# Optimization experiments

Hardware: AMD Instinct MI355X
Metric: run time of the kernel (lower is better)

Reference implementation:

```python
import jax, jax.numpy as jnp
import numpy as np

B = 2
L = 1024
D_MODEL = 1024
D_INNER = 2048   # expand * d_model
D_STATE = 16
DT_RANK = 64     # ceil(d_model / 16)
D_CONV = 4


def setup_inputs() -> dict:
    key = jax.random.key(0)
    ks = jax.random.split(key, 8)
    def nrm(k, shape, scale):
        return jax.random.normal(k, shape, dtype=jnp.float32) * scale
    A_log = jnp.log(jnp.tile(jnp.arange(1, D_STATE + 1, dtype=jnp.float32)[None, :], (D_INNER, 1)))
    return dict(
        hidden_states=jax.random.normal(ks[0], (B, L, D_MODEL), dtype=jnp.float32),
        Win=nrm(ks[1], (D_MODEL, 2 * D_INNER), D_MODEL ** -0.5),
        Wx=nrm(ks[2], (D_INNER, DT_RANK + 2 * D_STATE), D_INNER ** -0.5),
        Wdt=nrm(ks[3], (DT_RANK, D_INNER), DT_RANK ** -0.5),
        dt_bias=nrm(ks[4], (D_INNER,), 1.0),
        Wout=nrm(ks[5], (D_INNER, D_MODEL), D_INNER ** -0.5),
        dw_kernel=nrm(ks[6], (D_CONV, D_INNER), 0.2),
        dw_bias=jnp.zeros((D_INNER,), dtype=jnp.float32),
        A_log=A_log,
        Dskip=jnp.ones((D_INNER,), dtype=jnp.float32),
    )


def _causal_depthwise_conv(x, kernel, bias):
    # x: (B, L, D_INNER), kernel: (k, D_INNER); dilation 1, causal left pad
    k = kernel.shape[0]
    Lq = x.shape[1]
    xpad = jnp.pad(x, ((0, 0), (k - 1, 0), (0, 0)))
    y = sum(xpad[:, i:i + Lq, :] * kernel[i] for i in range(k)) + bias
    return jax.nn.silu(y)


def _selective_scan(u, delta, A, Bm, Cm, Dskip, z):
    # u, delta, z: (B, L, D); A: (D, N); Bm, Cm: (B, L, N)
    deltaA = jnp.exp(jnp.einsum('bld,dn->bldn', delta, A))      # (B,L,D,N)
    deltaBu = jnp.einsum('bld,bln,bld->bldn', delta, Bm, u)     # (B,L,D,N)

    def step(x_prev, elems):
        dA, dBu, c = elems                                      # (B,D,N),(B,D,N),(B,N)
        x_new = dA * x_prev + dBu
        y = jnp.einsum('bdn,bn->bd', x_new, c)
        return x_new, y

    x0 = jnp.zeros((u.shape[0], u.shape[2], A.shape[1]), dtype=jnp.float32)
    _, ys = jax.lax.scan(
        step, x0,
        (deltaA.transpose(1, 0, 2, 3), deltaBu.transpose(1, 0, 2, 3), Cm.transpose(1, 0, 2)))
    y = ys.transpose(1, 0, 2) + u * Dskip                        # skip connection
    return y * jax.nn.silu(z)


def reference(hidden_states, Win, Wx, Wdt, dt_bias, Wout, dw_kernel, dw_bias, A_log, Dskip):
    xz = hidden_states @ Win                                     # (B,L,2*D_INNER)
    x, z = jnp.split(xz, 2, axis=-1)
    A = -jnp.exp(A_log)                                          # (D_INNER, D_STATE)
    x = _causal_depthwise_conv(x, dw_kernel, dw_bias)
    x_dbl = x @ Wx                                               # (B,L,DT_RANK+2*N)
    dt, Bm, Cm = jnp.split(x_dbl, [DT_RANK, DT_RANK + D_STATE], axis=-1)
    delta = jax.nn.softplus(dt @ Wdt + dt_bias)                  # delta_bias + softplus
    y = _selective_scan(x, delta, A, Bm, Cm, Dskip, z)
    return y @ Wout
```

## Files before the change

### kernel.cpp

```cpp
#include <hip/hip_runtime.h>
#include <hip/hip_bf16.h>
#include <math.h>

#define B_SZ 2
#define L_SZ 1024
#define DM 1024
#define DI 2048
#define NS 16
#define DTR 64
#define NCHUNK 16
#define CLEN 64
#define XDLD 128
#define KSPLIT 16

typedef unsigned short ushortT;
typedef __attribute__((ext_vector_type(8))) short short8;
typedef __attribute__((ext_vector_type(4))) float floatx4;

__device__ __forceinline__ ushortT f2bf(float f) {
  unsigned u = __float_as_uint(f);
  unsigned r = (u + 0x7fff + ((u >> 16) & 1)) >> 16;
  return (ushortT)r;
}

__device__ __forceinline__ float bf2f(ushortT v) {
  return __uint_as_float((unsigned)v << 16);
}

__device__ __forceinline__ void gl2lds16(const void* g, void* l) {
  __builtin_amdgcn_global_load_lds(
      (const __attribute__((address_space(1))) unsigned int*)g,
      (__attribute__((address_space(3))) unsigned int*)l, 16, 0, 0);
}

__device__ __forceinline__ unsigned stash_addr(unsigned i) {
  return (i >> 10) * 4096 + 1024 + (i & 1023);
}

__global__ __launch_bounds__(256) void cvt_bf16(const float* __restrict__ src,
                                                ushortT* __restrict__ dst) {
  const int i = blockIdx.x * 256 + threadIdx.x;
  float4 v = ((const float4*)src)[i];
  unsigned lo = (unsigned)f2bf(v.x) | ((unsigned)f2bf(v.y) << 16);
  unsigned hi = (unsigned)f2bf(v.z) | ((unsigned)f2bf(v.w) << 16);
  ((uint2*)dst)[i] = make_uint2(lo, hi);
}

__global__ __launch_bounds__(256) void transpose_bf16(
    const float* __restrict__ src, ushortT* __restrict__ dst, int R, int C) {
  __shared__ float t[32][33];
  const int bx = blockIdx.x * 32;
  const int by = blockIdx.y * 32;
  const int tx = threadIdx.x, ty = threadIdx.y;
#pragma unroll
  for (int j = 0; j < 4; ++j)
    t[ty + j * 8][tx] = src[(size_t)(by + ty + j * 8) * C + bx + tx];
  __syncthreads();
#pragma unroll
  for (int j = 0; j < 4; ++j)
    dst[(size_t)(bx + ty + j * 8) * R + by + tx] = f2bf(t[tx][ty + j * 8]);
}

__global__ __launch_bounds__(256) void wx_pad_t(const float* __restrict__ Wx,
                                                ushortT* __restrict__ WxT) {
  const int k = blockIdx.x * 256 + threadIdx.x;
  const int n = blockIdx.y;
  WxT[(size_t)n * DI + k] = (n < 96) ? f2bf(Wx[(size_t)k * 96 + n]) : (ushortT)0;
}

__global__ __launch_bounds__(512) void gemm1_big(
    const ushortT* __restrict__ A, int lda,
    const ushortT* __restrict__ BT, int ldb,
    float* __restrict__ C, int ldc, int K) {
  __shared__ __align__(16) char smem[128 * 128 + 128 * 128];
  char* As = smem;
  char* Bs = smem + 128 * 128;
  const int tid = threadIdx.x;
  const int lane = tid & 63;
  const int quad = lane >> 4;
  const int l16 = lane & 15;
  const int wid = tid >> 6;
  const int wm = wid & 1;
  const int wn = wid >> 1;
  const int m0 = blockIdx.y * 128;
  const int n0 = blockIdx.x * 128;

  floatx4 acc[4][2] = {};

  for (int k0 = 0; k0 < K; k0 += 64) {
    for (int i = tid; i < 128 * 8; i += 512) {
      const int r = i >> 3, c = i & 7;
      const int cg = c ^ (r & 7);
      gl2lds16(A + (size_t)(m0 + r) * lda + k0 + cg * 8, As + (i - lane) * 16);
    }
    for (int i = tid; i < 128 * 8; i += 512) {
      const int r = i >> 3, c = i & 7;
      const int cg = c ^ (r & 7);
      gl2lds16(BT + (size_t)(n0 + r) * ldb + k0 + cg * 8, Bs + (i - lane) * 16);
    }
    __syncthreads();

    short8 afr[4][2], bfr[2][2];
#pragma unroll
    for (int i = 0; i < 4; ++i) {
      const int r = wm * 64 + i * 16 + l16;
#pragma unroll
      for (int s = 0; s < 2; ++s)
        afr[i][s] = *(const short8*)(As + r * 128 + (((s * 4 + quad) ^ (r & 7)) * 16));
    }
#pragma unroll
    for (int j = 0; j < 2; ++j) {
      const int r = wn * 32 + j * 16 + l16;
#pragma unroll
      for (int s = 0; s < 2; ++s)
        bfr[j][s] = *(const short8*)(Bs + r * 128 + (((s * 4 + quad) ^ (r & 7)) * 16));
    }
#pragma unroll
    for (int s = 0; s < 2; ++s)
#pragma unroll
      for (int i = 0; i < 4; ++i)
#pragma unroll
        for (int j = 0; j < 2; ++j)
          acc[i][j] = __builtin_amdgcn_mfma_f32_16x16x32_bf16(afr[i][s], bfr[j][s],
                                                              acc[i][j], 0, 0, 0);
    __syncthreads();
  }
#pragma unroll
  for (int i = 0; i < 4; ++i)
#pragma unroll
    for (int j = 0; j < 2; ++j)
#pragma unroll
      for (int r = 0; r < 4; ++r) {
        const int m = m0 + wm * 64 + i * 16 + quad * 4 + r;
        const int n = n0 + wn * 32 + j * 16 + l16;
        C[(size_t)m * ldc + n] = acc[i][j][r];
      }
}

__global__ __launch_bounds__(256) void gemm_out_split(
    const ushortT* __restrict__ A, int lda,
    const ushortT* __restrict__ BT, int ldb,
    float* __restrict__ part) {
  __shared__ __align__(16) char smem[64 * 128 + 64 * 128];
  char* As = smem;
  char* Bs = smem + 64 * 128;
  const int tid = threadIdx.x;
  const int lane = tid & 63;
  const int quad = lane >> 4;
  const int l16 = lane & 15;
  const int wid = tid >> 6;
  const int wm = wid & 1;
  const int wn = wid >> 1;
  const int m0 = blockIdx.y * 64;
  const int n0 = blockIdx.x * 64;
  const int kb = blockIdx.z * (DI / 2);

  floatx4 acc[2][2] = {};

  for (int k0 = kb; k0 < kb + DI / 2; k0 += 64) {
    for (int i = tid; i < 64 * 8; i += 256) {
      const int r = i >> 3, c = i & 7;
      const int cg = c ^ (r & 7);
      gl2lds16(A + (size_t)(m0 + r) * lda + k0 + cg * 8, As + (i - lane) * 16);
    }
    for (int i = tid; i < 64 * 8; i += 256) {
      const int r = i >> 3, c = i & 7;
      const int cg = c ^ (r & 7);
      gl2lds16(BT + (size_t)(n0 + r) * ldb + k0 + cg * 8, Bs + (i - lane) * 16);
    }
    __syncthreads();

    short8 afr[2][2], bfr[2][2];
#pragma unroll
    for (int i = 0; i < 2; ++i) {
      const int m = wm * 32 + i * 16 + l16;
#pragma unroll
      for (int s = 0; s < 2; ++s)
        afr[i][s] = *(const short8*)(As + m * 128 + (((s * 4 + quad) ^ (m & 7)) * 16));
    }
#pragma unroll
    for (int j = 0; j < 2; ++j) {
      const int n = wn * 32 + j * 16 + l16;
#pragma unroll
      for (int s = 0; s < 2; ++s)
        bfr[j][s] = *(const short8*)(Bs + n * 128 + (((s * 4 + quad) ^ (n & 7)) * 16));
    }
#pragma unroll
    for (int s = 0; s < 2; ++s)
#pragma unroll
      for (int i = 0; i < 2; ++i)
#pragma unroll
        for (int j = 0; j < 2; ++j)
          acc[i][j] = __builtin_amdgcn_mfma_f32_16x16x32_bf16(afr[i][s], bfr[j][s],
                                                              acc[i][j], 0, 0, 0);
    __syncthreads();
  }
  float* out = part + (size_t)blockIdx.z * (B_SZ * L_SZ * DM);
#pragma unroll
  for (int i = 0; i < 2; ++i)
#pragma unroll
    for (int j = 0; j < 2; ++j)
#pragma unroll
      for (int r = 0; r < 4; ++r) {
        const int m = m0 + wm * 32 + i * 16 + quad * 4 + r;
        const int n = n0 + wn * 32 + j * 16 + l16;
        out[(size_t)m * DM + n] = acc[i][j][r];
      }
}

__global__ __launch_bounds__(256) void reduce_out(const float* __restrict__ part,
                                                  float* __restrict__ out) {
  const int i = blockIdx.x * 256 + threadIdx.x;
  const float4 a = ((const float4*)part)[i];
  const float4 b = ((const float4*)part)[(size_t)(B_SZ * L_SZ * DM / 4) + i];
  ((float4*)out)[i] = make_float4(a.x + b.x, a.y + b.y, a.z + b.z, a.w + b.w);
}

__global__ __launch_bounds__(256) void gemm_xdbl_mfma(
    const ushortT* __restrict__ xcb, const ushortT* __restrict__ WxT,
    float* __restrict__ part) {
  __shared__ __align__(16) char smem[64 * 64 + 128 * 64];
  char* As = smem;
  char* Bs = smem + 64 * 64;
  const int tid = threadIdx.x;
  const int lane = tid & 63;
  const int quad = lane >> 4;
  const int l16 = lane & 15;
  const int wid = tid >> 6;
  const int wm = wid & 1;
  const int wn = wid >> 1;
  const int m0 = blockIdx.x * 64;
  const int kbase = blockIdx.y * (DI / KSPLIT);

  floatx4 acc[2][4] = {};

  for (int kk = 0; kk < DI / KSPLIT; kk += 32) {
    const int k0 = kbase + kk;
    for (int i = tid; i < 64 * 4; i += 256) {
      const int r = i >> 2, c = i & 3;
      const int cg = c ^ (r & 3);
      gl2lds16(xcb + (size_t)(m0 + r) * DI + k0 + cg * 8, As + (i - lane) * 16);
    }
    for (int i = tid; i < 128 * 4; i += 256) {
      const int r = i >> 2, c = i & 3;
      const int cg = c ^ (r & 3);
      gl2lds16(WxT + (size_t)r * DI + k0 + cg * 8, Bs + (i - lane) * 16);
    }
    __syncthreads();

    short8 afr[2], bfr[4];
#pragma unroll
    for (int i = 0; i < 2; ++i) {
      const int m = wm * 32 + i * 16 + l16;
      afr[i] = *(const short8*)(As + m * 64 + ((quad ^ (m & 3)) * 16));
    }
#pragma unroll
    for (int j = 0; j < 4; ++j) {
      const int n = wn * 64 + j * 16 + l16;
      bfr[j] = *(const short8*)(Bs + n * 64 + ((quad ^ (n & 3)) * 16));
    }
#pragma unroll
    for (int i = 0; i < 2; ++i)
#pragma unroll
      for (int j = 0; j < 4; ++j)
        acc[i][j] = __builtin_amdgcn_mfma_f32_16x16x32_bf16(afr[i], bfr[j],
                                                            acc[i][j], 0, 0, 0);
    __syncthreads();
  }
  float* out = part + (size_t)blockIdx.y * (B_SZ * L_SZ * XDLD);
#pragma unroll
  for (int i = 0; i < 2; ++i)
#pragma unroll
    for (int j = 0; j < 4; ++j)
#pragma unroll
      for (int r = 0; r < 4; ++r) {
        const int m = m0 + wm * 32 + i * 16 + quad * 4 + r;
        const int n = wn * 64 + j * 16 + l16;
        out[(size_t)m * XDLD + n] = acc[i][j][r];
      }
}

__global__ __launch_bounds__(256) void xdbl_reduce(const float* __restrict__ part,
                                                   float* __restrict__ xdbl,
                                                   ushortT* __restrict__ dtb) {
  const int i = blockIdx.x * 256 + threadIdx.x;
  float4 a = ((const float4*)part)[i];
#pragma unroll
  for (int s = 1; s < KSPLIT; ++s) {
    const float4 b = ((const float4*)part)[(size_t)s * (B_SZ * L_SZ * XDLD / 4) + i];
    a.x += b.x; a.y += b.y; a.z += b.z; a.w += b.w;
  }
  ((float4*)xdbl)[i] = a;
  const int row = i >> 5;
  const int c4 = (i & 31) * 4;
  if (c4 < DTR) {
    const unsigned lo = (unsigned)f2bf(a.x) | ((unsigned)f2bf(a.y) << 16);
    const unsigned hi = (unsigned)f2bf(a.z) | ((unsigned)f2bf(a.w) << 16);
    ((uint2*)dtb)[row * (DTR / 4) + (c4 >> 2)] = make_uint2(lo, hi);
  }
}

__global__ __launch_bounds__(256) void conv_silu(
    const float* __restrict__ xz, const float* __restrict__ kern,
    const float* __restrict__ bias, ushortT* __restrict__ xcb) {
  const int d = blockIdx.y * 256 + threadIdx.x;
  const int b = blockIdx.x >> 7;
  const int l0 = (blockIdx.x & 127) * 8;
  const int row0 = b * L_SZ + l0;
  const float k0v = kern[0 * DI + d], k1v = kern[1 * DI + d];
  const float k2v = kern[2 * DI + d], k3v = kern[3 * DI + d];
  float xv[11];
#pragma unroll
  for (int i = 0; i < 11; ++i) {
    const int l = l0 - 3 + i;
    xv[i] = (l >= 0) ? xz[((size_t)(b * L_SZ + l)) * 4096 + d] : 0.f;
  }
  const float bs = bias[d];
#pragma unroll
  for (int j = 0; j < 8; ++j) {
    float a = bs;
    a = fmaf(xv[j], k0v, a);
    a = fmaf(xv[j + 1], k1v, a);
    a = fmaf(xv[j + 2], k2v, a);
    a = fmaf(xv[j + 3], k3v, a);
    xcb[(size_t)(row0 + j) * DI + d] = f2bf(a / (1.f + __expf(-a)));
  }
}

__global__ __launch_bounds__(256) void gemm_delta_mfma(
    const ushortT* __restrict__ dtb, const ushortT* __restrict__ WdtT,
    const float* __restrict__ dt_bias, float* __restrict__ delta) {
  __shared__ __align__(16) char smem[64 * 128 + 64 * 128];
  char* As = smem;
  char* Bs = smem + 64 * 128;
  const int tid = threadIdx.x;
  const int lane = tid & 63;
  const int quad = lane >> 4;
  const int l16 = lane & 15;
  const int wid = tid >> 6;
  const int wm = wid & 1;
  const int wn = wid >> 1;
  const int m0 = blockIdx.x * 64;
  const int n0 = blockIdx.y * 64;

  for (int i = tid; i < 64 * 8; i += 256) {
    const int r = i >> 3, c = i & 7;
    const int cg = c ^ (r & 7);
    gl2lds16(dtb + (size_t)(m0 + r) * DTR + cg * 8, As + (i - lane) * 16);
  }
  for (int i = tid; i < 64 * 8; i += 256) {
    const int r = i >> 3, c = i & 7;
    const int cg = c ^ (r & 7);
    gl2lds16(WdtT + (size_t)(n0 + r) * DTR + cg * 8, Bs + (i - lane) * 16);
  }
  __syncthreads();

  floatx4 acc[2][2] = {};
  short8 afr[2][2], bfr[2][2];
#pragma unroll
  for (int i = 0; i < 2; ++i) {
    const int m = wm * 32 + i * 16 + l16;
#pragma unroll
    for (int s = 0; s < 2; ++s)
      afr[i][s] = *(const short8*)(As + m * 128 + (((s * 4 + quad) ^ (m & 7)) * 16));
  }
#pragma unroll
  for (int j = 0; j < 2; ++j) {
    const int n = wn * 32 + j * 16 + l16;
#pragma unroll
    for (int s = 0; s < 2; ++s)
      bfr[j][s] = *(const short8*)(Bs + n * 128 + (((s * 4 + quad) ^ (n & 7)) * 16));
  }
#pragma unroll
  for (int s = 0; s < 2; ++s)
#pragma unroll
    for (int i = 0; i < 2; ++i)
#pragma unroll
      for (int j = 0; j < 2; ++j)
        acc[i][j] = __builtin_amdgcn_mfma_f32_16x16x32_bf16(afr[i][s], bfr[j][s],
                                                            acc[i][j], 0, 0, 0);

#pragma unroll
  for (int i = 0; i < 2; ++i)
#pragma unroll
    for (int j = 0; j < 2; ++j) {
      const int n = n0 + wn * 32 + j * 16 + l16;
      const float bias = dt_bias[n];
#pragma unroll
      for (int r = 0; r < 4; ++r) {
        const int m = m0 + wm * 32 + i * 16 + quad * 4 + r;
        const float a = acc[i][j][r] + bias;
        delta[(size_t)m * DI + n] = (a > 20.f) ? a : __logf(1.f + __expf(a));
      }
    }
}

__global__ __launch_bounds__(256) void scan_phase1(
    const float* __restrict__ delta, const ushortT* __restrict__ xcb,
    const float* __restrict__ xdbl, const float* __restrict__ A_log,
    float* __restrict__ xz) {
  const int bx = blockIdx.x;
  const int b = bx >> 9;
  const int c = (bx >> 5) & 15;
  const int dt = bx & 31;
  const int tid = threadIdx.x;
  const int dl = tid >> 2, nq = tid & 3;
  const int d = dt * 64 + dl;
  const int row0 = b * L_SZ + c * CLEN;

  __shared__ float Bsh[CLEN][16];
  for (int i = tid; i < CLEN * 16; i += 256)
    Bsh[i >> 4][i & 15] = xdbl[(size_t)(row0 + (i >> 4)) * XDLD + 64 + (i & 15)];

  float Av[4];
#pragma unroll
  for (int j = 0; j < 4; ++j) Av[j] = -__expf(A_log[d * 16 + nq * 4 + j]);
  float x[4] = {}, P[4] = {1.f, 1.f, 1.f, 1.f};
  __syncthreads();

  const float* dp = delta + (size_t)row0 * DI + d;
  const ushortT* up = xcb + (size_t)row0 * DI + d;
  float dB[4], uB[4];
#pragma unroll
  for (int j = 0; j < 4; ++j) {
    dB[j] = dp[(size_t)j * DI];
    uB[j] = bf2f(up[(size_t)j * DI]);
  }
  for (int l0 = 0; l0 < CLEN; l0 += 4) {
    float dN[4] = {}, uN[4] = {};
    if (l0 + 4 < CLEN) {
#pragma unroll
      for (int j = 0; j < 4; ++j) {
        dN[j] = dp[(size_t)(l0 + 4 + j) * DI];
        uN[j] = bf2f(up[(size_t)(l0 + 4 + j) * DI]);
      }
    }
#pragma unroll
    for (int jj = 0; jj < 4; ++jj) {
      const float dlt = dB[jj];
      const float t = dlt * uB[jj];
      const float* bb = &Bsh[l0 + jj][nq * 4];
#pragma unroll
      for (int n = 0; n < 4; ++n) {
        const float dA = __expf(dlt * Av[n]);
        P[n] *= dA;
        x[n] = fmaf(dA, x[n], t * bb[n]);
      }
    }
#pragma unroll
    for (int j = 0; j < 4; ++j) { dB[j] = dN[j]; uB[j] = uN[j]; }
  }
  const unsigned sb = ((unsigned)((b * NCHUNK + c) * DI + d)) * 16 + nq * 4;
  *(float4*)&xz[stash_addr(sb)] = make_float4(P[0], P[1], P[2], P[3]);
  *(float4*)&xz[stash_addr((1u << 20) + sb)] = make_float4(x[0], x[1], x[2], x[3]);
}

__global__ __launch_bounds__(256) void scan_phase2(float* __restrict__ xz) {
  const int t = blockIdx.x * 256 + threadIdx.x;
  const int b = t >> 15;
  const int rem = t & 32767;
  float x = 0.f;
#pragma unroll
  for (int c = 0; c < NCHUNK; ++c) {
    const unsigned i = ((unsigned)(b * NCHUNK + c) << 15) + rem;
    float* Pr = &xz[stash_addr(i)];
    float* Sr = &xz[stash_addr((1u << 20) + i)];
    const float P = *Pr, S = *Sr;
    *Sr = x;
    x = fmaf(P, x, S);
  }
}

__global__ __launch_bounds__(256) void scan_phase3(
    const float* __restrict__ delta, const ushortT* __restrict__ xcb,
    const float* __restrict__ xdbl, const float* __restrict__ A_log,
    const float* __restrict__ Dskip, float* __restrict__ xz) {
  const int bx = blockIdx.x;
  const int b = bx >> 9;
  const int c = (bx >> 5) & 15;
  const int dt = bx & 31;
  const int tid = threadIdx.x;
  const int dl = tid >> 2, nq = tid & 3;
  const int d = dt * 64 + dl;
  const int row0 = b * L_SZ + c * CLEN;

  __shared__ float Bsh[CLEN][16], Csh[CLEN][16];
  for (int i = tid; i < CLEN * 32; i += 256) {
    const int r = i >> 5, q = i & 31;
    const float v = xdbl[(size_t)(row0 + r) * XDLD + 64 + q];
    if (q < 16) Bsh[r][q] = v; else Csh[r][q - 16] = v;
  }

  float Av[4];
#pragma unroll
  for (int j = 0; j < 4; ++j) Av[j] = -__expf(A_log[d * 16 + nq * 4 + j]);
  const float Dsk = Dskip[d];
  const unsigned sb = ((unsigned)((b * NCHUNK + c) * DI + d)) * 16 + nq * 4;
  const float4 xi = *(const float4*)&xz[stash_addr((1u << 20) + sb)];
  float x[4] = {xi.x, xi.y, xi.z, xi.w};
  __syncthreads();

  const float* dp = delta + (size_t)row0 * DI + d;
  const ushortT* up = xcb + (size_t)row0 * DI + d;
  const float* zp = xz + (size_t)row0 * 4096 + DI + d;
  ushortT* yb = (ushortT*)xz;

  float dB[4], uB[4], zB[4];
#pragma unroll
  for (int j = 0; j < 4; ++j) {
    dB[j] = dp[(size_t)j * DI];
    uB[j] = bf2f(up[(size_t)j * DI]);
    zB[j] = zp[(size_t)j * 4096];
  }
  for (int l0 = 0; l0 < CLEN; l0 += 4) {
    float dN[4] = {}, uN[4] = {}, zN[4] = {};
    if (l0 + 4 < CLEN) {
#pragma unroll
      for (int j = 0; j < 4; ++j) {
        dN[j] = dp[(size_t)(l0 + 4 + j) * DI];
        uN[j] = bf2f(up[(size_t)(l0 + 4 + j) * DI]);
        zN[j] = zp[(size_t)(l0 + 4 + j) * 4096];
      }
    }
#pragma unroll
    for (int jj = 0; jj < 4; ++jj) {
      const float dlt = dB[jj];
      const float u = uB[jj];
      const float t = dlt * u;
      const float* bb = &Bsh[l0 + jj][nq * 4];
      const float* cc = &Csh[l0 + jj][nq * 4];
      float y = 0.f;
#pragma unroll
      for (int n = 0; n < 4; ++n) {
        const float dA = __expf(dlt * Av[n]);
        x[n] = fmaf(dA, x[n], t * bb[n]);
        y = fmaf(x[n], cc[n], y);
      }
      y += __shfl_xor(y, 1);
      y += __shfl_xor(y, 2);
      if (nq == 0) {
        const float z = zB[jj];
        const float g = (y + u * Dsk) * (z / (1.f + __expf(-z)));
        yb[(size_t)(row0 + l0 + jj) * 8192 + d] = f2bf(g);
      }
    }
#pragma unroll
    for (int j = 0; j < 4; ++j) { dB[j] = dN[j]; uB[j] = uN[j]; zB[j] = zN[j]; }
  }
}

extern "C" void kernel_launch(void* const* d_in, const int* in_sizes, int n_in,
                              void* d_out, int out_size, void* d_ws, size_t ws_size,
                              hipStream_t stream) {
  const float* hidden  = (const float*)d_in[0];
  const float* Win     = (const float*)d_in[1];
  const float* Wx      = (const float*)d_in[2];
  const float* Wdt     = (const float*)d_in[3];
  const float* dt_bias = (const float*)d_in[4];
  const float* Wout    = (const float*)d_in[5];
  const float* dwk     = (const float*)d_in[6];
  const float* dwb     = (const float*)d_in[7];
  const float* A_log   = (const float*)d_in[8];
  const float* Dskip   = (const float*)d_in[9];

  char* ws = (char*)d_ws;
  float* xz       = (float*)ws;
  float* shared16 = (float*)(ws + (32u << 20));
  float* xcreg    = (float*)(ws + (48u << 20));
  ushortT* xcb    = (ushortT*)xcreg;
  char* dob = (char*)d_out;
  ushortT* hidb = (ushortT*)dob;
  float* xdbl   = (float*)(dob + (4u << 20));
  ushortT* WxT  = (ushortT*)(dob + (5u << 20));
  ushortT* WdtT = (ushortT*)(dob + (5u << 20) + (512u << 10));
  ushortT* dtb  = (ushortT*)(dob + (5u << 20) + (768u << 10));

  cvt_bf16<<<dim3(B_SZ * L_SZ * DM / 1024), 256, 0, stream>>>(hidden, hidb);
  transpose_bf16<<<dim3(4096 / 32, 1024 / 32), dim3(32, 8), 0, stream>>>(
      Win, (ushortT*)shared16, DM, 2 * DI);
  wx_pad_t<<<dim3(DI / 256, 128), 256, 0, stream>>>(Wx, WxT);
  transpose_bf16<<<dim3(DI / 32, DTR / 32), dim3(32, 8), 0, stream>>>(
      Wdt, WdtT, DTR, DI);
  gemm1_big<<<dim3(4096 / 128, 2048 / 128), 512, 0, stream>>>(
      hidb, DM, (ushortT*)shared16, DM, xz, 2 * DI, DM);
  conv_silu<<<dim3(B_SZ * L_SZ / 8, DI / 256), 256, 0, stream>>>(xz, dwk, dwb, xcb);
  gemm_xdbl_mfma<<<dim3(B_SZ * L_SZ / 64, KSPLIT), 256, 0, stream>>>(
      xcb, WxT, shared16);
  xdbl_reduce<<<dim3(B_SZ * L_SZ * XDLD / 1024), 256, 0, stream>>>(shared16, xdbl, dtb);
  gemm_delta_mfma<<<dim3(B_SZ * L_SZ / 64, DI / 64), 256, 0, stream>>>(
      dtb, WdtT, dt_bias, shared16);
  scan_phase1<<<dim3(B_SZ * NCHUNK * (DI / 64)), 256, 0, stream>>>(
      shared16, xcb, xdbl, A_log, xz);
  scan_phase2<<<dim3(B_SZ * DI * NS / 256), 256, 0, stream>>>(xz);
  scan_phase3<<<dim3(B_SZ * NCHUNK * (DI / 64)), 256, 0, stream>>>(
      shared16, xcb, xdbl, A_log, Dskip, xz);
  transpose_bf16<<<dim3(1024 / 32, 2048 / 32), dim3(32, 8), 0, stream>>>(
      Wout, (ushortT*)shared16, DI, DM);
  gemm_out_split<<<dim3(1024 / 64, 2048 / 64, 2), 256, 0, stream>>>(
      (ushortT*)xz, 4 * DI, (ushortT*)shared16, DI, xcreg);
  reduce_out<<<dim3(B_SZ * L_SZ * DM / 1024), 256, 0, stream>>>(xcreg, (float*)d_out);
}
```

Measured before the change: 239.4 us.

## Fuse prep kernels, drop scan phase2 and out-GEMM split-K reduction

Merges the bf16 conversion and all weight transposes, including Wout, into one prep_all launch. Removes scan_phase2 by having each scan_phase3 block fold the preceding chunk carries itself, and replaces the split-K output GEMM plus reduce with a single full-K GEMM that writes straight to the output. Halves KSPLIT for the xdbl GEMM. The goal is fewer launches and less partial-sum traffic, at the cost of redundant carry work in phase3 and lower parallelism in the output GEMM.

```diff
diff --git a/kernel.cpp b/kernel.cpp
--- a/kernel.cpp
+++ b/kernel.cpp
@@ -11,7 +11,7 @@
 #define NCHUNK 16
 #define CLEN 64
 #define XDLD 128
-#define KSPLIT 16
+#define KSPLIT 8
 
 typedef unsigned short ushortT;
 typedef __attribute__((ext_vector_type(8))) short short8;
@@ -37,21 +37,10 @@
   return (i >> 10) * 4096 + 1024 + (i & 1023);
 }
 
-__global__ __launch_bounds__(256) void cvt_bf16(const float* __restrict__ src,
-                                                ushortT* __restrict__ dst) {
-  const int i = blockIdx.x * 256 + threadIdx.x;
-  float4 v = ((const float4*)src)[i];
-  unsigned lo = (unsigned)f2bf(v.x) | ((unsigned)f2bf(v.y) << 16);
-  unsigned hi = (unsigned)f2bf(v.z) | ((unsigned)f2bf(v.w) << 16);
-  ((uint2*)dst)[i] = make_uint2(lo, hi);
-}
-
-__global__ __launch_bounds__(256) void transpose_bf16(
-    const float* __restrict__ src, ushortT* __restrict__ dst, int R, int C) {
-  __shared__ float t[32][33];
-  const int bx = blockIdx.x * 32;
-  const int by = blockIdx.y * 32;
-  const int tx = threadIdx.x, ty = threadIdx.y;
+__device__ __forceinline__ void tr_body(const float* __restrict__ src,
+                                        ushortT* __restrict__ dst, int R, int C,
+                                        int bx, int by, int tx, int ty,
+                                        float (*t)[33]) {
 #pragma unroll
   for (int j = 0; j < 4; ++j)
     t[ty + j * 8][tx] = src[(size_t)(by + ty + j * 8) * C + bx + tx];
@@ -61,11 +50,37 @@
     dst[(size_t)(bx + ty + j * 8) * R + by + tx] = f2bf(t[tx][ty + j * 8]);
 }
 
-__global__ __launch_bounds__(256) void wx_pad_t(const float* __restrict__ Wx,
-                                                ushortT* __restrict__ WxT) {
-  const int k = blockIdx.x * 256 + threadIdx.x;
-  const int n = blockIdx.y;
-  WxT[(size_t)n * DI + k] = (n < 96) ? f2bf(Wx[(size_t)k * 96 + n]) : (ushortT)0;
+__global__ __launch_bounds__(256) void prep_all(
+    const float* __restrict__ hidden, ushortT* __restrict__ hidb,
+    const float* __restrict__ Win, ushortT* __restrict__ WinT,
+    const float* __restrict__ Wx, ushortT* __restrict__ WxT,
+    const float* __restrict__ Wdt, ushortT* __restrict__ WdtT,
+    const float* __restrict__ Wout, ushortT* __restrict__ WoutT) {
+  __shared__ float t[32][33];
+  const int blk = blockIdx.x;
+  const int tid = threadIdx.x;
+  const int tx = tid & 31, ty = tid >> 5;
+  if (blk < 2048) {
+    const int i = blk * 256 + tid;
+    float4 v = ((const float4*)hidden)[i];
+    unsigned lo = (unsigned)f2bf(v.x) | ((unsigned)f2bf(v.y) << 16);
+    unsigned hi = (unsigned)f2bf(v.z) | ((unsigned)f2bf(v.w) << 16);
+    ((uint2*)hidb)[i] = make_uint2(lo, hi);
+  } else if (blk < 6144) {
+    const int rel = blk - 2048;
+    tr_body(Win, WinT, DM, 2 * DI, (rel & 127) * 32, (rel >> 7) * 32, tx, ty, t);
+  } else if (blk < 7168) {
+    const int rel = blk - 6144;
+    const int k = (rel & 7) * 256 + tid;
+    const int n = rel >> 3;
+    WxT[(size_t)n * DI + k] = (n < 96) ? f2bf(Wx[(size_t)k * 96 + n]) : (ushortT)0;
+  } else if (blk < 7296) {
+    const int rel = blk - 7168;
+    tr_body(Wdt, WdtT, DTR, DI, (rel & 63) * 32, (rel >> 6) * 32, tx, ty, t);
+  } else {
+    const int rel = blk - 7296;
+    tr_body(Wout, WoutT, DI, DM, (rel & 31) * 32, (rel >> 5) * 32, tx, ty, t);
+  }
 }
 
 __global__ __launch_bounds__(512) void gemm1_big(
@@ -137,10 +152,10 @@
       }
 }
 
-__global__ __launch_bounds__(256) void gemm_out_split(
+__global__ __launch_bounds__(256) void gemm_out(
     const ushortT* __restrict__ A, int lda,
     const ushortT* __restrict__ BT, int ldb,
-    float* __restrict__ part) {
+    float* __restrict__ C) {
   __shared__ __align__(16) char smem[64 * 128 + 64 * 128];
   char* As = smem;
   char* Bs = smem + 64 * 128;
@@ -153,11 +168,10 @@
   const int wn = wid >> 1;
   const int m0 = blockIdx.y * 64;
   const int n0 = blockIdx.x * 64;
-  const int kb = blockIdx.z * (DI / 2);
 
   floatx4 acc[2][2] = {};
 
-  for (int k0 = kb; k0 < kb + DI / 2; k0 += 64) {
+  for (int k0 = 0; k0 < DI; k0 += 64) {
     for (int i = tid; i < 64 * 8; i += 256) {
       const int r = i >> 3, c = i & 7;
       const int cg = c ^ (r & 7);
@@ -195,7 +209,6 @@
                                                               acc[i][j], 0, 0, 0);
     __syncthreads();
   }
-  float* out = part + (size_t)blockIdx.z * (B_SZ * L_SZ * DM);
 #pragma unroll
   for (int i = 0; i < 2; ++i)
 #pragma unroll
@@ -204,16 +217,8 @@
       for (int r = 0; r < 4; ++r) {
         const int m = m0 + wm * 32 + i * 16 + quad * 4 + r;
         const int n = n0 + wn * 32 + j * 16 + l16;
-        out[(size_t)m * DM + n] = acc[i][j][r];
-      }
-}
-
-__global__ __launch_bounds__(256) void reduce_out(const float* __restrict__ part,
-                                                  float* __restrict__ out) {
-  const int i = blockIdx.x * 256 + threadIdx.x;
-  const float4 a = ((const float4*)part)[i];
-  const float4 b = ((const float4*)part)[(size_t)(B_SZ * L_SZ * DM / 4) + i];
-  ((float4*)out)[i] = make_float4(a.x + b.x, a.y + b.y, a.z + b.z, a.w + b.w);
+        C[(size_t)m * DM + n] = acc[i][j][r];
+      }
 }
 
 __global__ __launch_bounds__(256) void gemm_xdbl_mfma(
@@ -455,22 +460,6 @@
   *(float4*)&xz[stash_addr((1u << 20) + sb)] = make_float4(x[0], x[1], x[2], x[3]);
 }
 
-__global__ __launch_bounds__(256) void scan_phase2(float* __restrict__ xz) {
-  const int t = blockIdx.x * 256 + threadIdx.x;
-  const int b = t >> 15;
-  const int rem = t & 32767;
-  float x = 0.f;
-#pragma unroll
-  for (int c = 0; c < NCHUNK; ++c) {
-    const unsigned i = ((unsigned)(b * NCHUNK + c) << 15) + rem;
-    float* Pr = &xz[stash_addr(i)];
-    float* Sr = &xz[stash_addr((1u << 20) + i)];
-    const float P = *Pr, S = *Sr;
-    *Sr = x;
-    x = fmaf(P, x, S);
-  }
-}
-
 __global__ __launch_bounds__(256) void scan_phase3(
     const float* __restrict__ delta, const ushortT* __restrict__ xcb,
     const float* __restrict__ xdbl, const float* __restrict__ A_log,
@@ -495,9 +484,17 @@
 #pragma unroll
   for (int j = 0; j < 4; ++j) Av[j] = -__expf(A_log[d * 16 + nq * 4 + j]);
   const float Dsk = Dskip[d];
-  const unsigned sb = ((unsigned)((b * NCHUNK + c) * DI + d)) * 16 + nq * 4;
-  const float4 xi = *(const float4*)&xz[stash_addr((1u << 20) + sb)];
-  float x[4] = {xi.x, xi.y, xi.z, xi.w};
+
+  float x[4] = {0.f, 0.f, 0.f, 0.f};
+  for (int cc = 0; cc < c; ++cc) {
+    const unsigned ib = ((unsigned)((b * NCHUNK + cc) * DI + d)) * 16 + nq * 4;
+    const float4 P = *(const float4*)&xz[stash_addr(ib)];
+    const float4 S = *(const float4*)&xz[stash_addr((1u << 20) + ib)];
+    x[0] = fmaf(P.x, x[0], S.x);
+    x[1] = fmaf(P.y, x[1], S.y);
+    x[2] = fmaf(P.z, x[2], S.z);
+    x[3] = fmaf(P.w, x[3], S.w);
+  }
   __syncthreads();
 
   const float* dp = delta + (size_t)row0 * DI + d;
@@ -566,8 +563,8 @@
   char* ws = (char*)d_ws;
   float* xz       = (float*)ws;
   float* shared16 = (float*)(ws + (32u << 20));
-  float* xcreg    = (float*)(ws + (48u << 20));
-  ushortT* xcb    = (ushortT*)xcreg;
+  ushortT* xcb    = (ushortT*)(ws + (48u << 20));
+  ushortT* WoutT  = (ushortT*)(ws + (56u << 20));
   char* dob = (char*)d_out;
   ushortT* hidb = (ushortT*)dob;
   float* xdbl   = (float*)(dob + (4u << 20));
@@ -575,12 +572,8 @@
   ushortT* WdtT = (ushortT*)(dob + (5u << 20) + (512u << 10));
   ushortT* dtb  = (ushortT*)(dob + (5u << 20) + (768u << 10));
 
-  cvt_bf16<<<dim3(B_SZ * L_SZ * DM / 1024), 256, 0, stream>>>(hidden, hidb);
-  transpose_bf16<<<dim3(4096 / 32, 1024 / 32), dim3(32, 8), 0, stream>>>(
-      Win, (ushortT*)shared16, DM, 2 * DI);
-  wx_pad_t<<<dim3(DI / 256, 128), 256, 0, stream>>>(Wx, WxT);
-  transpose_bf16<<<dim3(DI / 32, DTR / 32), dim3(32, 8), 0, stream>>>(
-      Wdt, WdtT, DTR, DI);
+  prep_all<<<dim3(9344), 256, 0, stream>>>(hidden, hidb, Win, (ushortT*)shared16,
+                                           Wx, WxT, Wdt, WdtT, Wout, WoutT);
   gemm1_big<<<dim3(4096 / 128, 2048 / 128), 512, 0, stream>>>(
       hidb, DM, (ushortT*)shared16, DM, xz, 2 * DI, DM);
   conv_silu<<<dim3(B_SZ * L_SZ / 8, DI / 256), 256, 0, stream>>>(xz, dwk, dwb, xcb);
@@ -591,12 +584,8 @@
       dtb, WdtT, dt_bias, shared16);
   scan_phase1<<<dim3(B_SZ * NCHUNK * (DI / 64)), 256, 0, stream>>>(
       shared16, xcb, xdbl, A_log, xz);
-  scan_phase2<<<dim3(B_SZ * DI * NS / 256), 256, 0, stream>>>(xz);
   scan_phase3<<<dim3(B_SZ * NCHUNK * (DI / 64)), 256, 0, stream>>>(
       shared16, xcb, xdbl, A_log, Dskip, xz);
-  transpose_bf16<<<dim3(1024 / 32, 2048 / 32), dim3(32, 8), 0, stream>>>(
-      Wout, (ushortT*)shared16, DI, DM);
-  gemm_out_split<<<dim3(1024 / 64, 2048 / 64, 2), 256, 0, stream>>>(
-      (ushortT*)xz, 4 * DI, (ushortT*)shared16, DI, xcreg);
-  reduce_out<<<dim3(B_SZ * L_SZ * DM / 1024), 256, 0, stream>>>(xcreg, (float*)d_out);
-}
+  gemm_out<<<dim3(DM / 64, 2048 / 64), 256, 0, stream>>>(
+      (ushortT*)xz, 4 * DI, WoutT, DI, (float*)d_out);
+}
```

Result: faster. 231.7 us (-3.2%).
